# Kernel optimization log

Hardware: AMD Instinct MI355X
Metric: run time of the kernel (lower is better)

Reference implementation:

```python
import jax, jax.numpy as jnp
from jax import lax
import numpy as np

B, T, D = 16, 4096, 512          # batch, encoder length, d_model
C, FW = 10, 100                  # aconv_chans, aconv_filts (kernel width 2*FW+1)
SHARP = 2.0                      # sharpening_factor


def setup_inputs() -> dict:
    key = jax.random.key(0)
    ks = jax.random.split(key, 11)
    s = 1.0 / np.sqrt(D)
    sc = 1.0 / np.sqrt(2 * FW + 1)
    return {
        "value": jax.random.normal(ks[0], (B, T, D), jnp.float32),
        "query": jax.random.normal(ks[1], (B, D), jnp.float32),
        "input_lengths": jax.random.randint(ks[2], (B,), T // 2, T + 1),
        "att_prev": jax.random.uniform(ks[3], (B, T), jnp.float32),
        # learned parameters (torch Linear stores W as [out,in]; y = x @ W.T + b)
        "W_enc": jax.random.uniform(ks[4], (D, D), jnp.float32, -s, s),
        "b_enc": jax.random.uniform(ks[5], (D,), jnp.float32, -s, s),
        "W_dec": jax.random.uniform(ks[6], (D, D), jnp.float32, -s, s),
        "W_att": jax.random.uniform(ks[7], (D, C), jnp.float32, -s, s),
        "W_conv": jax.random.uniform(ks[8], (C, 1, 2 * FW + 1), jnp.float32, -sc, sc),
        "w_g": jax.random.uniform(ks[9], (1, D), jnp.float32, -s, s),
        "b_g": jax.random.uniform(ks[10], (1,), jnp.float32, -s, s),
    }


def reference(value, query, input_lengths, att_prev,
              W_enc, b_enc, W_dec, W_att, W_conv, w_g, b_g):
    # pre_compute_enc_h = mlp_enc(enc_h): [B,T,D]
    pre_enc = jnp.einsum('btd,ed->bte', value, W_enc) + b_enc
    # dec_z_tiled = mlp_dec(dec_z): [B,1,D]
    dec_tiled = (query @ W_dec.T)[:, None, :]
    # loc_conv: 1D conv over T, in_ch=1 -> out_ch=C, same padding -> [B,C,T]
    conv = lax.conv_general_dilated(att_prev[:, None, :], W_conv,
                                    window_strides=(1,), padding=[(FW, FW)],
                                    dimension_numbers=('NCH', 'OIH', 'NCH'))
    # mlp_att on transposed conv: [B,T,C] @ W_att.T -> [B,T,D]
    att_conv = jnp.einsum('bct,dc->btd', conv, W_att)
    # e = gvec(tanh(sum)): [B,T]
    e = jnp.einsum('btd,d->bt', jnp.tanh(att_conv + pre_enc + dec_tiled), w_g[0]) + b_g[0]
    # pad mask: positions >= length are masked to -inf (use large finite neg)
    pad_mask = jnp.arange(T)[None, :] >= input_lengths[:, None]
    e = jnp.where(pad_mask, -1e30, e)
    att_weights = jax.nn.softmax(SHARP * e, axis=1)            # [B,T]
    context = jnp.einsum('btd,bt->bd', value, att_weights)     # [B,D]
    return context, att_weights
```

## Files before the change

kernel.cpp:

```cpp
#include <hip/hip_runtime.h>
#include <hip/hip_bf16.h>

constexpr int kB  = 16;
constexpr int kT  = 4096;
constexpr int kD  = 512;
constexpr int kC  = 10;
constexpr int kFW = 100;
constexpr int kKW = 2 * kFW + 1;
constexpr int kKP = 544;
constexpr int kCP = 16;

typedef __attribute__((ext_vector_type(8))) short short8_t;
typedef __attribute__((ext_vector_type(4))) float float4_t;

__device__ __forceinline__ float tanh_fast(float x) {
  float ax = fabsf(x);
  float z  = __expf(-2.0f * ax);
  float r  = (1.0f - z) / (1.0f + z);
  return copysignf(r, x);
}

__device__ __forceinline__ short f2bf(float x) {
  unsigned u = __float_as_uint(x);
  u += 0x7fffu + ((u >> 16) & 1u);
  return (short)(u >> 16);
}

__device__ __forceinline__ void glds16(const void* g, void* l) {
  __builtin_amdgcn_global_load_lds(
      (const __attribute__((address_space(1))) void*)g,
      (__attribute__((address_space(3))) void*)l, 16, 0, 0);
}

__global__ void dec_bias_kernel(const float* __restrict__ query,
                                const float* __restrict__ W_dec,
                                const float* __restrict__ b_enc,
                                float* __restrict__ bias) {
  int gw   = (blockIdx.x * blockDim.x + threadIdx.x) >> 6;
  int lane = threadIdx.x & 63;
  int b = gw >> 9;
  int d = gw & (kD - 1);
  const float* q = query + (size_t)b * kD;
  const float* w = W_dec + (size_t)d * kD;
  float s = 0.f;
#pragma unroll
  for (int k0 = 0; k0 < kD; k0 += 256) {
    float4 qa = *(const float4*)(q + k0 + lane * 4);
    float4 wa = *(const float4*)(w + k0 + lane * 4);
    s += qa.x * wa.x + qa.y * wa.y + qa.z * wa.z + qa.w * wa.w;
  }
#pragma unroll
  for (int off = 32; off > 0; off >>= 1) s += __shfl_down(s, off, 64);
  if (lane == 0) bias[gw] = b_enc[d] + s;
}

__global__ void pack_w_kernel(const float* __restrict__ W_enc,
                              const float* __restrict__ W_att,
                              short* __restrict__ Wbf) {
  int d = blockIdx.x;
  for (int c = threadIdx.x; c < kKP; c += 256) {
    float v = 0.f;
    if (c < kD)            v = W_enc[(size_t)d * kD + c];
    else if (c < kD + kC)  v = W_att[(size_t)d * kC + (c - kD)];
    Wbf[(size_t)d * kKP + c] = f2bf(v);
  }
}

__global__ void conv_kernel(const float* __restrict__ att_prev,
                            const float* __restrict__ W_conv,
                            float* __restrict__ convT16) {
  __shared__ float ap[256 + 2 * kFW];
  __shared__ float wc[kC * kKW];
  int b   = blockIdx.y;
  int t0  = blockIdx.x * 256;
  int tid = threadIdx.x;
  for (int i = tid; i < kC * kKW; i += 256) wc[i] = W_conv[i];
  for (int i = tid; i < 256 + 2 * kFW; i += 256) {
    int p = t0 - kFW + i;
    ap[i] = (p >= 0 && p < kT) ? att_prev[(size_t)b * kT + p] : 0.f;
  }
  __syncthreads();
  float acc[kC];
#pragma unroll
  for (int c = 0; c < kC; ++c) acc[c] = 0.f;
  for (int j = 0; j < kKW; ++j) {
    float a = ap[tid + j];
#pragma unroll
    for (int c = 0; c < kC; ++c) acc[c] += a * wc[c * kKW + j];
  }
  float* out = convT16 + ((size_t)b * kT + t0 + tid) * kCP;
#pragma unroll
  for (int c = 0; c < kC; ++c) out[c] = acc[c];
#pragma unroll
  for (int c = kC; c < kCP; ++c) out[c] = 0.f;
}

constexpr int BM = 128, BN = 128, BK = 32;

__global__ __launch_bounds__(256) void e_kernel(
    const float* __restrict__ value, const float* __restrict__ convT16,
    const short* __restrict__ Wbf, const float* __restrict__ bias,
    const float* __restrict__ w_g, const int* __restrict__ lens,
    float* __restrict__ e_buf) {
  __shared__ short As[BM][40];
  __shared__ short Bs[BM * BK];

  int tid = threadIdx.x;
  int L    = blockIdx.x;
  int xcd  = L & 7;
  int slot = L >> 3;
  int bn   = slot & 3;
  int mt   = xcd * 64 + (slot >> 2);
  int b  = mt >> 5;
  int t0 = (mt & 31) * BM;
  if (t0 >= lens[b]) return;
  int n0 = bn * BN;

  int w    = tid >> 6;
  int lane = tid & 63;
  int nl   = lane & 15;
  int quad = lane >> 4;
  int wm = w >> 1, wn = w & 1;

  int srow = tid >> 1, skh = tid & 1;
  const float* aptr = value + ((size_t)(b * kT + t0) + srow) * kD + skh * 16;
  const float* cptr = convT16 + ((size_t)(b * kT + t0) + srow) * kCP;

  const short* bptr0 = Wbf + (size_t)(n0 + w * 32 + (lane >> 2)) * kKP + (lane & 3) * 8;
  const short* bptr1 = bptr0 + (size_t)16 * kKP;
  short* bs0 = &Bs[(w * 32) * BK];
  short* bs1 = &Bs[(w * 32 + 16) * BK];

  float4_t acc[4][4] = {};

  for (int kk = 0; kk < 17; ++kk) {
    int k0 = kk * BK;
    __syncthreads();
    glds16(bptr0 + k0, bs0);
    glds16(bptr1 + k0, bs1);
    short av[16];
    if (kk < 16) {
      float4 f0 = *(const float4*)(aptr + k0);
      float4 f1 = *(const float4*)(aptr + k0 + 4);
      float4 f2 = *(const float4*)(aptr + k0 + 8);
      float4 f3 = *(const float4*)(aptr + k0 + 12);
      av[0] = f2bf(f0.x); av[1] = f2bf(f0.y); av[2]  = f2bf(f0.z); av[3]  = f2bf(f0.w);
      av[4] = f2bf(f1.x); av[5] = f2bf(f1.y); av[6]  = f2bf(f1.z); av[7]  = f2bf(f1.w);
      av[8] = f2bf(f2.x); av[9] = f2bf(f2.y); av[10] = f2bf(f2.z); av[11] = f2bf(f2.w);
      av[12] = f2bf(f3.x); av[13] = f2bf(f3.y); av[14] = f2bf(f3.z); av[15] = f2bf(f3.w);
    } else if (skh == 0) {
      float4 f0 = *(const float4*)(cptr);
      float4 f1 = *(const float4*)(cptr + 4);
      float4 f2 = *(const float4*)(cptr + 8);
      float4 f3 = *(const float4*)(cptr + 12);
      av[0] = f2bf(f0.x); av[1] = f2bf(f0.y); av[2]  = f2bf(f0.z); av[3]  = f2bf(f0.w);
      av[4] = f2bf(f1.x); av[5] = f2bf(f1.y); av[6]  = f2bf(f1.z); av[7]  = f2bf(f1.w);
      av[8] = f2bf(f2.x); av[9] = f2bf(f2.y); av[10] = f2bf(f2.z); av[11] = f2bf(f2.w);
      av[12] = f2bf(f3.x); av[13] = f2bf(f3.y); av[14] = f2bf(f3.z); av[15] = f2bf(f3.w);
    } else {
#pragma unroll
      for (int i = 0; i < 16; ++i) av[i] = 0;
    }
    *(short8_t*)(&As[srow][skh * 16])     = *(short8_t*)(&av[0]);
    *(short8_t*)(&As[srow][skh * 16 + 8]) = *(short8_t*)(&av[8]);
    __syncthreads();

    short8_t a_frag[4], b_frag[4];
#pragma unroll
    for (int i = 0; i < 4; ++i)
      a_frag[i] = *(const short8_t*)(&As[wm * 64 + i * 16 + nl][quad * 8]);
#pragma unroll
    for (int j = 0; j < 4; ++j)
      b_frag[j] = *(const short8_t*)(&Bs[(wn * 64 + j * 16 + nl) * BK + quad * 8]);
#pragma unroll
    for (int i = 0; i < 4; ++i)
#pragma unroll
      for (int j = 0; j < 4; ++j)
        acc[i][j] = __builtin_amdgcn_mfma_f32_16x16x32_bf16(
            a_frag[i], b_frag[j], acc[i][j], 0, 0, 0);
  }

  float bias_r[4], wg_r[4];
#pragma unroll
  for (int j = 0; j < 4; ++j) {
    int d = n0 + wn * 64 + j * 16 + nl;
    bias_r[j] = bias[b * kD + d];
    wg_r[j]   = w_g[d];
  }
#pragma unroll
  for (int i = 0; i < 4; ++i) {
#pragma unroll
    for (int r = 0; r < 4; ++r) {
      float s = 0.f;
#pragma unroll
      for (int j = 0; j < 4; ++j)
        s += wg_r[j] * tanh_fast(acc[i][j][r] + bias_r[j]);
      s += __shfl_xor(s, 1, 64);
      s += __shfl_xor(s, 2, 64);
      s += __shfl_xor(s, 4, 64);
      s += __shfl_xor(s, 8, 64);
      if (nl == 0) {
        int t = t0 + wm * 64 + i * 16 + quad * 4 + r;
        atomicAdd(&e_buf[(size_t)b * kT + t], s);
      }
    }
  }
}

__global__ void softmax_kernel(const float* __restrict__ e_buf,
                               const int* __restrict__ lens,
                               float* __restrict__ att) {
  __shared__ float sred[256];
  int b = blockIdx.x, tid = threadIdx.x;
  int len = lens[b];
  const float* e = e_buf + (size_t)b * kT;
  float m = -3.0e38f;
  for (int t = tid; t < len; t += 256) m = fmaxf(m, e[t]);
  sred[tid] = m; __syncthreads();
  for (int s = 128; s > 0; s >>= 1) {
    if (tid < s) sred[tid] = fmaxf(sred[tid], sred[tid + s]);
    __syncthreads();
  }
  m = sred[0]; __syncthreads();
  float sum = 0.f;
  for (int t = tid; t < len; t += 256) sum += __expf(2.0f * (e[t] - m));
  sred[tid] = sum; __syncthreads();
  for (int s = 128; s > 0; s >>= 1) {
    if (tid < s) sred[tid] += sred[tid + s];
    __syncthreads();
  }
  float inv = 1.0f / sred[0];
  for (int t = tid; t < kT; t += 256)
    att[(size_t)b * kT + t] = (t < len) ? __expf(2.0f * (e[t] - m)) * inv : 0.0f;
}

__global__ void context_kernel(const float* __restrict__ value,
                               const float* __restrict__ att,
                               const int* __restrict__ lens,
                               float* __restrict__ ctx) {
  int b = blockIdx.y;
  int len = lens[b];
  int t0 = blockIdx.x * 128;
  if (t0 >= len) return;
  int tid = threadIdx.x;
  int d4 = (tid & 127) * 4;
  int th = tid >> 7;
  int tb = t0 + th * 64;
  int tmax = min(64, len - tb);
  const float* ap = att + (size_t)b * kT + tb;
  const float* vp = value + ((size_t)(b * kT) + tb) * kD + d4;
  float4 a = {0.f, 0.f, 0.f, 0.f};
  for (int t = 0; t < tmax; ++t) {
    float wt = ap[t];
    float4 v = *(const float4*)(vp + (size_t)t * kD);
    a.x += wt * v.x; a.y += wt * v.y; a.z += wt * v.z; a.w += wt * v.w;
  }
  if (tmax > 0) {
    atomicAdd(&ctx[b * kD + d4],     a.x);
    atomicAdd(&ctx[b * kD + d4 + 1], a.y);
    atomicAdd(&ctx[b * kD + d4 + 2], a.z);
    atomicAdd(&ctx[b * kD + d4 + 3], a.w);
  }
}

extern "C" void kernel_launch(void* const* d_in, const int* in_sizes, int n_in,
                              void* d_out, int out_size, void* d_ws, size_t ws_size,
                              hipStream_t stream) {
  const float* value    = (const float*)d_in[0];
  const float* query    = (const float*)d_in[1];
  const int*   lens     = (const int*)  d_in[2];
  const float* att_prev = (const float*)d_in[3];
  const float* W_enc    = (const float*)d_in[4];
  const float* b_enc    = (const float*)d_in[5];
  const float* W_dec    = (const float*)d_in[6];
  const float* W_att    = (const float*)d_in[7];
  const float* W_conv   = (const float*)d_in[8];
  const float* w_g      = (const float*)d_in[9];

  float* ws      = (float*)d_ws;
  float* e_buf   = ws;
  float* convT16 = ws + (size_t)kB * kT;
  float* bias    = convT16 + (size_t)kB * kT * kCP;
  short* Wbf     = (short*)(bias + (size_t)kB * kD);
  float* ctx = (float*)d_out;
  float* att = ctx + (size_t)kB * kD;

  hipMemsetAsync(e_buf, 0, (size_t)kB * kT * sizeof(float), stream);
  hipMemsetAsync(ctx,   0, (size_t)kB * kD * sizeof(float), stream);

  dec_bias_kernel<<<kB * kD / 4, 256, 0, stream>>>(query, W_dec, b_enc, bias);
  pack_w_kernel<<<kD, 256, 0, stream>>>(W_enc, W_att, Wbf);
  conv_kernel<<<dim3(kT / 256, kB), 256, 0, stream>>>(att_prev, W_conv, convT16);
  e_kernel<<<2048, 256, 0, stream>>>(value, convT16, Wbf, bias, w_g, lens, e_buf);
  softmax_kernel<<<kB, 256, 0, stream>>>(e_buf, lens, att);
  context_kernel<<<dim3(kT / 128, kB), 256, 0, stream>>>(value, att, lens, ctx);
}
```

Baseline: 314.7 us.

## Swizzle GEMM LDS tiles, prefetch A, bf16 conv staging, drop e atomics

The e_kernel GEMM now uses XOR-swizzled LDS layouts for both the A and B tiles instead of padded rows, and prefetches the next A tile from global memory into registers during the MFMA step. The conv output is written as bf16 and loaded straight into LDS with global_load_lds. The atomicAdd accumulation of e is replaced by plain stores into 8 partial buffers that the softmax kernel sums and caches in shared memory, which also removes a memset. The aim is fewer LDS bank conflicts, less global load latency on the GEMM critical path, and no atomic contention, at the cost of a larger workspace and extra partial-sum reads in softmax.

```diff
diff --git a/kernel.cpp b/kernel.cpp
--- a/kernel.cpp
+++ b/kernel.cpp
@@ -8,7 +8,7 @@
 constexpr int kFW = 100;
 constexpr int kKW = 2 * kFW + 1;
 constexpr int kKP = 544;
-constexpr int kCP = 16;
+constexpr int kCW = 32;
 
 typedef __attribute__((ext_vector_type(8))) short short8_t;
 typedef __attribute__((ext_vector_type(4))) float float4_t;
@@ -24,6 +24,11 @@
   unsigned u = __float_as_uint(x);
   u += 0x7fffu + ((u >> 16) & 1u);
   return (short)(u >> 16);
+}
+
+__device__ __forceinline__ unsigned pk2(float lo, float hi) {
+  __hip_bfloat162 h = __float22bfloat162_rn(make_float2(lo, hi));
+  union { __hip_bfloat162 h2; unsigned u; } cv; cv.h2 = h; return cv.u;
 }
 
 __device__ __forceinline__ void glds16(const void* g, void* l) {
@@ -68,7 +73,7 @@
 
 __global__ void conv_kernel(const float* __restrict__ att_prev,
                             const float* __restrict__ W_conv,
-                            float* __restrict__ convT16) {
+                            short* __restrict__ convbf) {
   __shared__ float ap[256 + 2 * kFW];
   __shared__ float wc[kC * kKW];
   int b   = blockIdx.y;
@@ -88,22 +93,27 @@
 #pragma unroll
     for (int c = 0; c < kC; ++c) acc[c] += a * wc[c * kKW + j];
   }
-  float* out = convT16 + ((size_t)b * kT + t0 + tid) * kCP;
-#pragma unroll
-  for (int c = 0; c < kC; ++c) out[c] = acc[c];
-#pragma unroll
-  for (int c = kC; c < kCP; ++c) out[c] = 0.f;
+  unsigned ow[16];
+#pragma unroll
+  for (int i = 0; i < 5; ++i) ow[i] = pk2(acc[2 * i], acc[2 * i + 1]);
+#pragma unroll
+  for (int i = 5; i < 16; ++i) ow[i] = 0u;
+  uint4* out = (uint4*)(convbf + ((size_t)b * kT + t0 + tid) * kCW);
+  out[0] = make_uint4(ow[0], ow[1], ow[2], ow[3]);
+  out[1] = make_uint4(ow[4], ow[5], ow[6], ow[7]);
+  out[2] = make_uint4(ow[8], ow[9], ow[10], ow[11]);
+  out[3] = make_uint4(ow[12], ow[13], ow[14], ow[15]);
 }
 
 constexpr int BM = 128, BN = 128, BK = 32;
 
 __global__ __launch_bounds__(256) void e_kernel(
-    const float* __restrict__ value, const float* __restrict__ convT16,
+    const float* __restrict__ value, const short* __restrict__ convbf,
     const short* __restrict__ Wbf, const float* __restrict__ bias,
     const float* __restrict__ w_g, const int* __restrict__ lens,
-    float* __restrict__ e_buf) {
-  __shared__ short As[BM][40];
-  __shared__ short Bs[BM * BK];
+    float* __restrict__ e_part) {
+  __shared__ short As[BM * BK];
+  __shared__ short Bs[BN * BK];
 
   int tid = threadIdx.x;
   int L    = blockIdx.x;
@@ -123,55 +133,60 @@
   int wm = w >> 1, wn = w & 1;
 
   int srow = tid >> 1, skh = tid & 1;
+  int ga = (srow >> 1) & 3;
   const float* aptr = value + ((size_t)(b * kT + t0) + srow) * kD + skh * 16;
-  const float* cptr = convT16 + ((size_t)(b * kT + t0) + srow) * kCP;
-
-  const short* bptr0 = Wbf + (size_t)(n0 + w * 32 + (lane >> 2)) * kKP + (lane & 3) * 8;
-  const short* bptr1 = bptr0 + (size_t)16 * kKP;
-  short* bs0 = &Bs[(w * 32) * BK];
-  short* bs1 = &Bs[(w * 32 + 16) * BK];
+  short* aw0 = &As[((srow << 2) + ((skh * 2)     ^ ga)) * 8];
+  short* aw1 = &As[((srow << 2) + ((skh * 2 + 1) ^ ga)) * 8];
+
+  int kps = (lane & 3) ^ ((lane >> 3) & 3);
+  const short* bsrc0 = Wbf + (size_t)(n0 + w * 32 + (lane >> 2)) * kKP + kps * 8;
+  const short* bsrc1 = bsrc0 + (size_t)16 * kKP;
+  short* bdst0 = &Bs[(w * 32) * BK];
+  short* bdst1 = &Bs[(w * 32 + 16) * BK];
+
+  const short* csrc0 = convbf + ((size_t)(b * kT + t0) + w * 32 + (lane >> 2)) * kCW + kps * 8;
+  const short* csrc1 = csrc0 + (size_t)16 * kCW;
+
+  int swz = quad ^ ((nl >> 1) & 3);
+  const short8_t* ard = (const short8_t*)&As[(((wm * 64 + nl) << 2) + swz) * 8];
+  const short8_t* brd = (const short8_t*)&Bs[(((wn * 64 + nl) << 2) + swz) * 8];
 
   float4_t acc[4][4] = {};
 
+  float4 pf0 = *(const float4*)(aptr);
+  float4 pf1 = *(const float4*)(aptr + 4);
+  float4 pf2 = *(const float4*)(aptr + 8);
+  float4 pf3 = *(const float4*)(aptr + 12);
+
   for (int kk = 0; kk < 17; ++kk) {
-    int k0 = kk * BK;
     __syncthreads();
-    glds16(bptr0 + k0, bs0);
-    glds16(bptr1 + k0, bs1);
-    short av[16];
+    glds16(bsrc0 + kk * BK, bdst0);
+    glds16(bsrc1 + kk * BK, bdst1);
     if (kk < 16) {
-      float4 f0 = *(const float4*)(aptr + k0);
-      float4 f1 = *(const float4*)(aptr + k0 + 4);
-      float4 f2 = *(const float4*)(aptr + k0 + 8);
-      float4 f3 = *(const float4*)(aptr + k0 + 12);
-      av[0] = f2bf(f0.x); av[1] = f2bf(f0.y); av[2]  = f2bf(f0.z); av[3]  = f2bf(f0.w);
-      av[4] = f2bf(f1.x); av[5] = f2bf(f1.y); av[6]  = f2bf(f1.z); av[7]  = f2bf(f1.w);
-      av[8] = f2bf(f2.x); av[9] = f2bf(f2.y); av[10] = f2bf(f2.z); av[11] = f2bf(f2.w);
-      av[12] = f2bf(f3.x); av[13] = f2bf(f3.y); av[14] = f2bf(f3.z); av[15] = f2bf(f3.w);
-    } else if (skh == 0) {
-      float4 f0 = *(const float4*)(cptr);
-      float4 f1 = *(const float4*)(cptr + 4);
-      float4 f2 = *(const float4*)(cptr + 8);
-      float4 f3 = *(const float4*)(cptr + 12);
-      av[0] = f2bf(f0.x); av[1] = f2bf(f0.y); av[2]  = f2bf(f0.z); av[3]  = f2bf(f0.w);
-      av[4] = f2bf(f1.x); av[5] = f2bf(f1.y); av[6]  = f2bf(f1.z); av[7]  = f2bf(f1.w);
-      av[8] = f2bf(f2.x); av[9] = f2bf(f2.y); av[10] = f2bf(f2.z); av[11] = f2bf(f2.w);
-      av[12] = f2bf(f3.x); av[13] = f2bf(f3.y); av[14] = f2bf(f3.z); av[15] = f2bf(f3.w);
+      union { short8_t s8; unsigned u[4]; } c0, c1;
+      c0.u[0] = pk2(pf0.x, pf0.y); c0.u[1] = pk2(pf0.z, pf0.w);
+      c0.u[2] = pk2(pf1.x, pf1.y); c0.u[3] = pk2(pf1.z, pf1.w);
+      c1.u[0] = pk2(pf2.x, pf2.y); c1.u[1] = pk2(pf2.z, pf2.w);
+      c1.u[2] = pk2(pf3.x, pf3.y); c1.u[3] = pk2(pf3.z, pf3.w);
+      *(short8_t*)aw0 = c0.s8;
+      *(short8_t*)aw1 = c1.s8;
     } else {
-#pragma unroll
-      for (int i = 0; i < 16; ++i) av[i] = 0;
+      glds16(csrc0, (void*)&As[(w * 32) * BK]);
+      glds16(csrc1, (void*)&As[(w * 32 + 16) * BK]);
     }
-    *(short8_t*)(&As[srow][skh * 16])     = *(short8_t*)(&av[0]);
-    *(short8_t*)(&As[srow][skh * 16 + 8]) = *(short8_t*)(&av[8]);
     __syncthreads();
-
+    if (kk < 15) {
+      const float* np = aptr + (kk + 1) * BK;
+      pf0 = *(const float4*)(np);
+      pf1 = *(const float4*)(np + 4);
+      pf2 = *(const float4*)(np + 8);
+      pf3 = *(const float4*)(np + 12);
+    }
     short8_t a_frag[4], b_frag[4];
 #pragma unroll
-    for (int i = 0; i < 4; ++i)
-      a_frag[i] = *(const short8_t*)(&As[wm * 64 + i * 16 + nl][quad * 8]);
-#pragma unroll
-    for (int j = 0; j < 4; ++j)
-      b_frag[j] = *(const short8_t*)(&Bs[(wn * 64 + j * 16 + nl) * BK + quad * 8]);
+    for (int i = 0; i < 4; ++i) a_frag[i] = ard[i * 64];
+#pragma unroll
+    for (int j = 0; j < 4; ++j) b_frag[j] = brd[j * 64];
 #pragma unroll
     for (int i = 0; i < 4; ++i)
 #pragma unroll
@@ -187,6 +202,8 @@
     bias_r[j] = bias[b * kD + d];
     wg_r[j]   = w_g[d];
   }
+  int p = wn * 4 + bn;
+  float* ep = e_part + ((size_t)p * kB + b) * kT + t0 + wm * 64;
 #pragma unroll
   for (int i = 0; i < 4; ++i) {
 #pragma unroll
@@ -199,23 +216,27 @@
       s += __shfl_xor(s, 2, 64);
       s += __shfl_xor(s, 4, 64);
       s += __shfl_xor(s, 8, 64);
-      if (nl == 0) {
-        int t = t0 + wm * 64 + i * 16 + quad * 4 + r;
-        atomicAdd(&e_buf[(size_t)b * kT + t], s);
-      }
+      if (nl == 0) ep[i * 16 + quad * 4 + r] = s;
     }
   }
 }
 
-__global__ void softmax_kernel(const float* __restrict__ e_buf,
+__global__ void softmax_kernel(const float* __restrict__ e_part,
                                const int* __restrict__ lens,
                                float* __restrict__ att) {
+  __shared__ float eb[kT];
   __shared__ float sred[256];
   int b = blockIdx.x, tid = threadIdx.x;
   int len = lens[b];
-  const float* e = e_buf + (size_t)b * kT;
+  const float* ep = e_part + (size_t)b * kT;
   float m = -3.0e38f;
-  for (int t = tid; t < len; t += 256) m = fmaxf(m, e[t]);
+  for (int t = tid; t < len; t += 256) {
+    float s = 0.f;
+#pragma unroll
+    for (int p = 0; p < 8; ++p) s += ep[(size_t)p * kB * kT + t];
+    eb[t] = s;
+    m = fmaxf(m, s);
+  }
   sred[tid] = m; __syncthreads();
   for (int s = 128; s > 0; s >>= 1) {
     if (tid < s) sred[tid] = fmaxf(sred[tid], sred[tid + s]);
@@ -223,7 +244,7 @@
   }
   m = sred[0]; __syncthreads();
   float sum = 0.f;
-  for (int t = tid; t < len; t += 256) sum += __expf(2.0f * (e[t] - m));
+  for (int t = tid; t < len; t += 256) sum += __expf(2.0f * (eb[t] - m));
   sred[tid] = sum; __syncthreads();
   for (int s = 128; s > 0; s >>= 1) {
     if (tid < s) sred[tid] += sred[tid + s];
@@ -231,7 +252,7 @@
   }
   float inv = 1.0f / sred[0];
   for (int t = tid; t < kT; t += 256)
-    att[(size_t)b * kT + t] = (t < len) ? __expf(2.0f * (e[t] - m)) * inv : 0.0f;
+    att[(size_t)b * kT + t] = (t < len) ? __expf(2.0f * (eb[t] - m)) * inv : 0.0f;
 }
 
 __global__ void context_kernel(const float* __restrict__ value,
@@ -250,6 +271,7 @@
   const float* ap = att + (size_t)b * kT + tb;
   const float* vp = value + ((size_t)(b * kT) + tb) * kD + d4;
   float4 a = {0.f, 0.f, 0.f, 0.f};
+#pragma unroll 4
   for (int t = 0; t < tmax; ++t) {
     float wt = ap[t];
     float4 v = *(const float4*)(vp + (size_t)t * kD);
@@ -277,21 +299,20 @@
   const float* W_conv   = (const float*)d_in[8];
   const float* w_g      = (const float*)d_in[9];
 
-  float* ws      = (float*)d_ws;
-  float* e_buf   = ws;
-  float* convT16 = ws + (size_t)kB * kT;
-  float* bias    = convT16 + (size_t)kB * kT * kCP;
-  short* Wbf     = (short*)(bias + (size_t)kB * kD);
+  float* ws     = (float*)d_ws;
+  float* e_part = ws;
+  short* convbf = (short*)(ws + (size_t)8 * kB * kT);
+  float* bias   = (float*)(convbf + (size_t)kB * kT * kCW);
+  short* Wbf    = (short*)(bias + (size_t)kB * kD);
   float* ctx = (float*)d_out;
   float* att = ctx + (size_t)kB * kD;
 
-  hipMemsetAsync(e_buf, 0, (size_t)kB * kT * sizeof(float), stream);
-  hipMemsetAsync(ctx,   0, (size_t)kB * kD * sizeof(float), stream);
+  hipMemsetAsync(ctx, 0, (size_t)kB * kD * sizeof(float), stream);
 
   dec_bias_kernel<<<kB * kD / 4, 256, 0, stream>>>(query, W_dec, b_enc, bias);
   pack_w_kernel<<<kD, 256, 0, stream>>>(W_enc, W_att, Wbf);
-  conv_kernel<<<dim3(kT / 256, kB), 256, 0, stream>>>(att_prev, W_conv, convT16);
-  e_kernel<<<2048, 256, 0, stream>>>(value, convT16, Wbf, bias, w_g, lens, e_buf);
-  softmax_kernel<<<kB, 256, 0, stream>>>(e_buf, lens, att);
+  conv_kernel<<<dim3(kT / 256, kB), 256, 0, stream>>>(att_prev, W_conv, convbf);
+  e_kernel<<<2048, 256, 0, stream>>>(value, convbf, Wbf, bias, w_g, lens, e_part);
+  softmax_kernel<<<kB, 256, 0, stream>>>(e_part, lens, att);
   context_kernel<<<dim3(kT / 128, kB), 256, 0, stream>>>(value, att, lens, ctx);
 }
```

Result: slower. 348.8 us (+10.8%).
